# Optimization experiments

Hardware: AMD Instinct MI355X
Metric: run time of the kernel (lower is better)

## Reference

```python
import jax, jax.numpy as jnp
import numpy as np
import math

N_HEADS = 16
N_KV_HEADS = 4
D_HEAD = 128
EPS = 1e-6
THETA = 10000.0


def _rmsnorm(x, w):
    var = jnp.mean(x * x, axis=-1, keepdims=True)
    return x * jax.lax.rsqrt(var + EPS) * w


def _rope_tables(S, dtype):
    freqs = 1.0 / THETA ** (jnp.arange(0, D_HEAD, 2, dtype=jnp.float32) / D_HEAD)
    angles = jnp.arange(S, dtype=jnp.float32)[:, None] * freqs[None, :]  # [S, D_HEAD/2]
    angles = jnp.concatenate([angles, angles], axis=-1)  # [S, D_HEAD]
    return jnp.cos(angles).astype(dtype), jnp.sin(angles).astype(dtype)


def _apply_rope(x, cos, sin):
    # x: [B, H, S, D]; rotate-half convention matching cat([angles, angles])
    half = D_HEAD // 2
    x1, x2 = x[..., :half], x[..., half:]
    rot = jnp.concatenate([-x2, x1], axis=-1)
    return x * cos[None, None] + rot * sin[None, None]


def setup_inputs() -> dict:
    key = jax.random.key(0)
    ks = jax.random.split(key, 5)
    B, S, D = 2, 2048, 2048
    s = 0.02
    return {
        "x": jax.random.normal(ks[0], (B, S, D), jnp.float32),
        "Wq": jax.random.normal(ks[1], (D, N_HEADS * D_HEAD), jnp.float32) * s,
        "Wk": jax.random.normal(ks[2], (D, N_KV_HEADS * D_HEAD), jnp.float32) * s,
        "Wv": jax.random.normal(ks[3], (D, N_KV_HEADS * D_HEAD), jnp.float32) * s,
        "Wo": jax.random.normal(ks[4], (D, D), jnp.float32) * s,
        "q_norm_w": jnp.ones((D_HEAD,), jnp.float32),
        "k_norm_w": jnp.ones((D_HEAD,), jnp.float32),
    }


def reference(x, Wq, Wk, Wv, Wo, q_norm_w, k_norm_w):
    B, S, D = x.shape
    groups = N_HEADS // N_KV_HEADS

    q = (x @ Wq).reshape(B, S, N_HEADS, D_HEAD).transpose(0, 2, 1, 3)      # [B,H,S,d]
    k = (x @ Wk).reshape(B, S, N_KV_HEADS, D_HEAD).transpose(0, 2, 1, 3)   # [B,Hkv,S,d]
    v = (x @ Wv).reshape(B, S, N_KV_HEADS, D_HEAD).transpose(0, 2, 1, 3)

    q = _rmsnorm(q, q_norm_w)
    k = _rmsnorm(k, k_norm_w)

    cos, sin = _rope_tables(S, x.dtype)
    q = _apply_rope(q, cos, sin)
    k = _apply_rope(k, cos, sin)

    # GQA broadcast: repeat kv heads into query head dim
    k = jnp.repeat(k, groups, axis=1)  # [B,H,S,d]
    v = jnp.repeat(v, groups, axis=1)

    scale = 1.0 / math.sqrt(D_HEAD)
    scores = jnp.einsum("bhqd,bhkd->bhqk", q, k) * scale
    causal = jnp.tril(jnp.ones((S, S), bool))
    scores = jnp.where(causal[None, None], scores, jnp.finfo(scores.dtype).min)
    probs = jax.nn.softmax(scores, axis=-1)
    out = jnp.einsum("bhqk,bhkd->bhqd", probs, v)  # [B,H,S,d]
    out = out.transpose(0, 2, 1, 3).reshape(B, S, D)
    return out @ Wo
```

## Files before the change

kernel.cpp:

```cpp
#include <hip/hip_runtime.h>
#include <stdint.h>

typedef __attribute__((ext_vector_type(8))) short bf16x8;
typedef __attribute__((ext_vector_type(4))) float f32x4;
typedef unsigned short u16;
typedef unsigned int   u32;

#define S_LEN 2048
#define NH    16
#define NKV   4
#define DH    128
#define DM    2048
#define QKV_N 3072
#define MROWS 4096

__device__ __forceinline__ u16 f2bf(float x) {
  u32 u = __float_as_uint(x);
  return (u16)((u + 0x7fffu + ((u >> 16) & 1u)) >> 16);
}
__device__ __forceinline__ float bf2f(u16 h) {
  return __uint_as_float(((u32)h) << 16);
}
__device__ __forceinline__ u32 cvtpk(float lo, float hi) {
  u32 r;
  asm("v_cvt_pk_bf16_f32 %0, %1, %2" : "=v"(r) : "v"(lo), "v"(hi));
  return r;
}
__device__ __forceinline__ void gload_lds16(const void* g, void* l) {
  __builtin_amdgcn_global_load_lds((const __attribute__((address_space(1))) void*)g,
                                   (__attribute__((address_space(3))) void*)l, 16, 0, 0);
}

__global__ void __launch_bounds__(256) convert_x_kernel(const float* __restrict__ x,
                                                        u16* __restrict__ o) {
  int idx = (blockIdx.x * 256 + threadIdx.x) * 8;
  float4 a = *(const float4*)(x + idx);
  float4 b = *(const float4*)(x + idx + 4);
  union { u16 s[8]; uint4 v; } t;
  t.s[0] = f2bf(a.x); t.s[1] = f2bf(a.y); t.s[2] = f2bf(a.z); t.s[3] = f2bf(a.w);
  t.s[4] = f2bf(b.x); t.s[5] = f2bf(b.y); t.s[6] = f2bf(b.z); t.s[7] = f2bf(b.w);
  *(uint4*)(o + idx) = t.v;
}

__global__ void __launch_bounds__(256) transpose_w_kernel(const float* __restrict__ src,
                                                          u16* __restrict__ dst, int N) {
  __shared__ float t[64][65];
  const int bx = blockIdx.x, by = blockIdx.y, tid = threadIdx.x;
#pragma unroll
  for (int rep = 0; rep < 16; ++rep) {
    int lin = rep * 256 + tid;
    int i = lin >> 6, jj = lin & 63;
    t[i][jj] = src[(size_t)(bx * 64 + i) * N + by * 64 + jj];
  }
  __syncthreads();
#pragma unroll
  for (int rep = 0; rep < 16; ++rep) {
    int lin = rep * 256 + tid;
    int nr = lin >> 6, kc = lin & 63;
    dst[(size_t)(by * 64 + nr) * DM + bx * 64 + kc] = f2bf(t[kc][nr]);
  }
}

__global__ void __launch_bounds__(256) rope_tables_kernel(float* __restrict__ ct,
                                                          float* __restrict__ st_) {
  int idx = blockIdx.x * 256 + threadIdx.x;
  int s = idx >> 6, i = idx & 63;
  const float L2_10000 = 13.287712379549449f;
  float freq = exp2f(-(float)i * (1.0f / 64.0f) * L2_10000);
  float ang = (float)s * freq;
  ct[idx] = cosf(ang);
  st_[idx] = sinf(ang);
}

template <int OUTF32>
__global__ void __launch_bounds__(256) gemm_bt(const u16* __restrict__ A,
                                               const u16* __restrict__ Bt,
                                               void* __restrict__ C,
                                               int M, int N, int K) {
  __shared__ __align__(16) u16 As[128 * 32];
  __shared__ __align__(16) u16 Bs[128 * 32];
  const int tid = threadIdx.x;
  const int w = tid >> 6, l = tid & 63;
  const int g = l >> 4, q15 = l & 15;
  const int row0 = blockIdx.y * 128, col0 = blockIdx.x * 128;
  const int wm = (w >> 1) * 64, wn = (w & 1) * 64;
  const f32x4 fz = {0.f, 0.f, 0.f, 0.f};
  f32x4 acc[4][4];
#pragma unroll
  for (int m = 0; m < 4; ++m)
#pragma unroll
    for (int n = 0; n < 4; ++n) acc[m][n] = fz;

  for (int kt = 0; kt < K; kt += 32) {
#pragma unroll
    for (int c = 0; c < 2; ++c) {
      int P = (w * 2 + c) * 1024;
      int Pl = P + l * 16;
      int arow = Pl >> 6, acolb = Pl & 63;
      gload_lds16((const char*)A + ((size_t)(row0 + arow) * K + kt) * 2 + acolb,
                  (char*)As + P);
      gload_lds16((const char*)Bt + ((size_t)(col0 + arow) * K + kt) * 2 + acolb,
                  (char*)Bs + P);
    }
    __syncthreads();
    bf16x8 af[4], bfv[4];
#pragma unroll
    for (int m = 0; m < 4; ++m)
      af[m] = *(const bf16x8*)((const char*)As + (wm + m * 16 + q15) * 64 + g * 16);
#pragma unroll
    for (int n = 0; n < 4; ++n)
      bfv[n] = *(const bf16x8*)((const char*)Bs + (wn + n * 16 + q15) * 64 + g * 16);
#pragma unroll
    for (int m = 0; m < 4; ++m)
#pragma unroll
      for (int n = 0; n < 4; ++n)
        acc[m][n] = __builtin_amdgcn_mfma_f32_16x16x32_bf16(af[m], bfv[n], acc[m][n], 0, 0, 0);
    __syncthreads();
  }
#pragma unroll
  for (int m = 0; m < 4; ++m)
#pragma unroll
    for (int n = 0; n < 4; ++n)
#pragma unroll
      for (int r = 0; r < 4; ++r) {
        int rr = row0 + wm + m * 16 + g * 4 + r;
        int cc = col0 + wn + n * 16 + q15;
        float v = acc[m][n][r];
        if (OUTF32) ((float*)C)[(size_t)rr * N + cc] = v;
        else        ((u16*)C)[(size_t)rr * N + cc]  = f2bf(v);
      }
}

__global__ void __launch_bounds__(256) norm_rope_kernel(const u16* __restrict__ qkv,
                                                        const float* __restrict__ qw,
                                                        const float* __restrict__ kw,
                                                        const float* __restrict__ ct,
                                                        const float* __restrict__ st_,
                                                        u16* __restrict__ Qo,
                                                        u16* __restrict__ Ko) {
  int wid = blockIdx.x * 4 + (threadIdx.x >> 6);
  int l = threadIdx.x & 63;
  int row = wid / 20;
  int j = wid - row * 20;
  int b = row >> 11, s = row & 2047;
  bool isq = j < 16;
  int h = isq ? j : (j - 16);
  const u16* src = qkv + (size_t)row * QKV_N + (isq ? h * DH : (2048 + h * DH));
  float x1 = bf2f(src[l]), x2 = bf2f(src[l + 64]);
  float ss = x1 * x1 + x2 * x2;
#pragma unroll
  for (int off = 32; off > 0; off >>= 1) ss += __shfl_xor(ss, off);
  float rn = rsqrtf(ss * (1.0f / 128.0f) + 1e-6f);
  const float* wv = isq ? qw : kw;
  float n1 = x1 * rn * wv[l], n2 = x2 * rn * wv[l + 64];
  float cv = ct[s * 64 + l], sv = st_[s * 64 + l];
  float o1 = n1 * cv - n2 * sv;
  float o2 = n2 * cv + n1 * sv;
  float scale = isq ? 0.08838834764831845f : 1.0f;
  u16* dst = isq ? (Qo + ((size_t)(b * NH + h) * S_LEN + s) * DH)
                 : (Ko + ((size_t)(b * NKV + h) * S_LEN + s) * DH);
  dst[l]      = f2bf(o1 * scale);
  dst[l + 64] = f2bf(o2 * scale);
}

__global__ void __launch_bounds__(256) vtrans_kernel(const u16* __restrict__ qkv,
                                                     u16* __restrict__ vt) {
  __shared__ u16 t[64][65];
  const int st = blockIdx.x, dt = blockIdx.y, bz = blockIdx.z;
  const int tid = threadIdx.x;
#pragma unroll
  for (int rep = 0; rep < 16; ++rep) {
    int lin = rep * 256 + tid;
    int i = lin >> 6, jj = lin & 63;
    t[i][jj] = qkv[(size_t)((bz >> 2) * S_LEN + st * 64 + i) * QKV_N
                   + 2560 + (bz & 3) * DH + dt * 64 + jj];
  }
  __syncthreads();
#pragma unroll
  for (int rep = 0; rep < 16; ++rep) {
    int lin = rep * 256 + tid;
    int dr = lin >> 6, sc = lin & 63;
    vt[((size_t)bz * DH + dt * 64 + dr) * S_LEN + st * 64 + sc] = t[sc][dr];
  }
}

__global__ void __launch_bounds__(512, 4) attn_kernel(const u16* __restrict__ Qg,
                                                      const u16* __restrict__ Kg,
                                                      const u16* __restrict__ Vt,
                                                      u16* __restrict__ O) {
  __shared__ __align__(16) char smem[65536];
  const int tid = threadIdx.x;
  const int w = tid >> 6, l = tid & 63;
  const int g = l >> 4, q15 = l & 15;
  const int id = blockIdx.x;
  const int grp = id & 7;
  const int mem = (id >> 3) & 3;
  const int tq  = 15 - (id >> 5);
  const int b   = grp >> 2, kvh = grp & 3;
  const int h   = kvh * 4 + mem;
  const int qb  = tq * 128;
  const int nkt = 2 * tq + 1;

  bf16x8 qreg[4];
  const u16* Qrow = Qg + ((size_t)(b * NH + h) * S_LEN + qb + w * 16 + q15) * DH;
#pragma unroll
  for (int c = 0; c < 4; ++c)
    qreg[c] = *(const bf16x8*)(Qrow + c * 32 + g * 8);

  const char* Kbase = (const char*)(Kg + (size_t)(b * NKV + kvh) * S_LEN * DH);
  const char* Vbase = (const char*)(Vt + (size_t)(b * NKV + kvh) * DH * S_LEN);

  auto stage = [&](int buf, int kt) {
    char* Ksb = smem + buf * 32768;
    if (w < 4) {
      const char* Kt = Kbase + (size_t)kt * 64 * 256;
#pragma unroll
      for (int i = 0; i < 4; ++i) {
        int off = w * 4096 + i * 1024 + l * 16;
        int row = off >> 8; int cb = (off & 255) ^ ((row & 7) << 4);
        gload_lds16(Kt + (size_t)row * 256 + cb, Ksb + off);
      }
    } else {
      const char* Vtb = Vbase + (size_t)kt * 128;
      char* Vsb = Ksb + 16384;
#pragma unroll
      for (int i = 0; i < 4; ++i) {
        int off = (w - 4) * 4096 + i * 1024 + l * 16;
        int row = off >> 7; int cb = (off & 127) ^ ((row & 7) << 4);
        gload_lds16(Vtb + (size_t)row * (S_LEN * 2) + cb, Vsb + off);
      }
    }
  };

  const f32x4 fz = {0.f, 0.f, 0.f, 0.f};
  f32x4 acc[8];
#pragma unroll
  for (int n = 0; n < 8; ++n) acc[n] = fz;
  float mrun = -1e30f, lrun = 0.f;

  stage(0, 0);
  __syncthreads();
  int cur = 0;

  for (int kt = 0; kt <= nkt; ++kt) {
    if (kt < nkt) stage(cur ^ 1, kt + 1);
    const char* Ks = smem + cur * 32768;
    const char* Vs = Ks + 16384;

    f32x4 sa[4];
#pragma unroll
    for (int stt = 0; stt < 4; ++stt) sa[stt] = fz;
    __builtin_amdgcn_s_setprio(1);
#pragma unroll
    for (int stt = 0; stt < 4; ++stt) {
      int krow = stt * 16 + q15;
      const char* kr = Ks + krow * 256;
      int sw = (krow & 7) << 4;
#pragma unroll
      for (int c = 0; c < 4; ++c) {
        bf16x8 kf = *(const bf16x8*)(kr + ((c * 64 + g * 16) ^ sw));
        sa[stt] = __builtin_amdgcn_mfma_f32_16x16x32_bf16(kf, qreg[c], sa[stt], 0, 0, 0);
      }
    }
    __builtin_amdgcn_s_setprio(0);

    const bool domask = (kt >= 2 * tq);
    float tmax = -1e30f;
#pragma unroll
    for (int stt = 0; stt < 4; ++stt)
#pragma unroll
      for (int r = 0; r < 4; ++r) {
        float v = sa[stt][r];
        if (domask) {
          int kvg = kt * 64 + stt * 16 + g * 4 + r;
          int qg  = qb + w * 16 + q15;
          if (kvg > qg) v = -1e30f;
        }
        sa[stt][r] = v;
        tmax = fmaxf(tmax, v);
      }
    tmax = fmaxf(tmax, __shfl_xor(tmax, 16));
    tmax = fmaxf(tmax, __shfl_xor(tmax, 32));

    const bool defer = __all(tmax <= mrun + 8.0f);
    float mnew = defer ? mrun : fmaxf(mrun, tmax);

    float tsum = 0.f;
    u32 pk[4][2];
#pragma unroll
    for (int stt = 0; stt < 4; ++stt) {
      float p0 = __expf(sa[stt][0] - mnew);
      float p1 = __expf(sa[stt][1] - mnew);
      float p2 = __expf(sa[stt][2] - mnew);
      float p3 = __expf(sa[stt][3] - mnew);
      tsum += p0 + p1 + p2 + p3;
      pk[stt][0] = cvtpk(p0, p1);
      pk[stt][1] = cvtpk(p2, p3);
    }
    tsum += __shfl_xor(tsum, 16);
    tsum += __shfl_xor(tsum, 32);

    if (defer) {
      lrun += tsum;
    } else {
      float alpha = __expf(mrun - mnew);
      lrun = lrun * alpha + tsum;
      mrun = mnew;
      float af4[4];
#pragma unroll
      for (int r = 0; r < 4; ++r) af4[r] = __shfl(alpha, g * 4 + r);
#pragma unroll
      for (int n = 0; n < 8; ++n) {
        f32x4 t = acc[n];
        t[0] *= af4[0]; t[1] *= af4[1]; t[2] *= af4[2]; t[3] *= af4[3];
        acc[n] = t;
      }
    }

#pragma unroll
    for (int c = 0; c < 2; ++c) {
      int srcA = ((2 * (g & 1)) << 4) | q15;
      int srcB = srcA + 16;
      u32 a00 = __shfl(pk[2 * c][0], srcA),     a01 = __shfl(pk[2 * c][1], srcA);
      u32 a02 = __shfl(pk[2 * c][0], srcB),     a03 = __shfl(pk[2 * c][1], srcB);
      u32 a10 = __shfl(pk[2 * c + 1][0], srcA), a11 = __shfl(pk[2 * c + 1][1], srcA);
      u32 a12 = __shfl(pk[2 * c + 1][0], srcB), a13 = __shfl(pk[2 * c + 1][1], srcB);
      bool hi = (g & 2) != 0;
      union { u32 u[4]; bf16x8 v; } afr;
      afr.u[0] = hi ? a10 : a00;
      afr.u[1] = hi ? a11 : a01;
      afr.u[2] = hi ? a12 : a02;
      afr.u[3] = hi ? a13 : a03;
      __builtin_amdgcn_s_setprio(1);
#pragma unroll
      for (int n = 0; n < 8; ++n) {
        int d = n * 16 + q15;
        const char* vr = Vs + d * 128;
        int sw = (d & 7) << 4;
        bf16x8 bv = *(const bf16x8*)(vr + ((c * 64 + g * 16) ^ sw));
        acc[n] = __builtin_amdgcn_mfma_f32_16x16x32_bf16(afr.v, bv, acc[n], 0, 0, 0);
      }
      __builtin_amdgcn_s_setprio(0);
    }
    __syncthreads();
    cur ^= 1;
  }

  float linv[4];
#pragma unroll
  for (int r = 0; r < 4; ++r) linv[r] = 1.0f / __shfl(lrun, g * 4 + r);
#pragma unroll
  for (int n = 0; n < 8; ++n)
#pragma unroll
    for (int r = 0; r < 4; ++r) {
      size_t orow = (size_t)b * S_LEN + qb + w * 16 + g * 4 + r;
      O[orow * DM + h * DH + n * 16 + q15] = f2bf(acc[n][r] * linv[r]);
    }
}

extern "C" void kernel_launch(void* const* d_in, const int* in_sizes, int n_in,
                              void* d_out, int out_size, void* d_ws, size_t ws_size,
                              hipStream_t stream) {
  (void)in_sizes; (void)n_in; (void)out_size; (void)ws_size;
  const float* x  = (const float*)d_in[0];
  const float* Wq = (const float*)d_in[1];
  const float* Wk = (const float*)d_in[2];
  const float* Wv = (const float*)d_in[3];
  const float* Wo = (const float*)d_in[4];
  const float* qw = (const float*)d_in[5];
  const float* kw = (const float*)d_in[6];

  char* ws = (char*)d_ws;
  u16*   xb    = (u16*)(ws + 0);
  u16*   wqkvt = (u16*)(ws + 16777216);
  u16*   wot   = (u16*)(ws + 29360128);
  u16*   qo    = (u16*)(ws + 37748736);
  u16*   ko    = (u16*)(ws + 54525952);
  u16*   vt    = (u16*)(ws + 58720256);
  float* ctab  = (float*)(ws + 62914560);
  float* stab  = (float*)(ws + 63438848);
  u16*   qkvp  = (u16*)d_out;
  u16*   attn  = (u16*)(ws + 0);
  float* outp  = (float*)d_out;

  convert_x_kernel<<<4096, 256, 0, stream>>>(x, xb);
  transpose_w_kernel<<<dim3(32, 32), 256, 0, stream>>>(Wq, wqkvt, 2048);
  transpose_w_kernel<<<dim3(32, 8),  256, 0, stream>>>(Wk, wqkvt + (size_t)2048 * 2048, 512);
  transpose_w_kernel<<<dim3(32, 8),  256, 0, stream>>>(Wv, wqkvt + (size_t)2560 * 2048, 512);
  transpose_w_kernel<<<dim3(32, 32), 256, 0, stream>>>(Wo, wot, 2048);
  rope_tables_kernel<<<512, 256, 0, stream>>>(ctab, stab);

  gemm_bt<0><<<dim3(24, 32), 256, 0, stream>>>(xb, wqkvt, qkvp, MROWS, QKV_N, DM);
  norm_rope_kernel<<<20480, 256, 0, stream>>>(qkvp, qw, kw, ctab, stab, qo, ko);
  vtrans_kernel<<<dim3(32, 2, 8), 256, 0, stream>>>(qkvp, vt);
  attn_kernel<<<512, 512, 0, stream>>>(qo, ko, vt, attn);
  gemm_bt<1><<<dim3(16, 32), 256, 0, stream>>>(attn, wot, outp, MROWS, DM, DM);
}
```

Baseline: 254.7 us.

## Process two 16-row query tiles per wave in attention, halving block threads

```diff
diff --git a/kernel.cpp b/kernel.cpp
--- a/kernel.cpp
+++ b/kernel.cpp
@@ -184,7 +184,7 @@
   }
 }
 
-__global__ void __launch_bounds__(512, 4) attn_kernel(const u16* __restrict__ Qg,
+__global__ void __launch_bounds__(256, 2) attn_kernel(const u16* __restrict__ Qg,
                                                       const u16* __restrict__ Kg,
                                                       const u16* __restrict__ Vt,
                                                       u16* __restrict__ O) {
@@ -201,42 +201,40 @@
   const int qb  = tq * 128;
   const int nkt = 2 * tq + 1;
 
-  bf16x8 qreg[4];
-  const u16* Qrow = Qg + ((size_t)(b * NH + h) * S_LEN + qb + w * 16 + q15) * DH;
-#pragma unroll
-  for (int c = 0; c < 4; ++c)
-    qreg[c] = *(const bf16x8*)(Qrow + c * 32 + g * 8);
+  bf16x8 qreg[2][4];
+#pragma unroll
+  for (int p = 0; p < 2; ++p) {
+    const u16* Qrow = Qg + ((size_t)(b * NH + h) * S_LEN + qb + w * 32 + p * 16 + q15) * DH;
+#pragma unroll
+    for (int c = 0; c < 4; ++c)
+      qreg[p][c] = *(const bf16x8*)(Qrow + c * 32 + g * 8);
+  }
 
   const char* Kbase = (const char*)(Kg + (size_t)(b * NKV + kvh) * S_LEN * DH);
   const char* Vbase = (const char*)(Vt + (size_t)(b * NKV + kvh) * DH * S_LEN);
 
   auto stage = [&](int buf, int kt) {
     char* Ksb = smem + buf * 32768;
-    if (w < 4) {
-      const char* Kt = Kbase + (size_t)kt * 64 * 256;
-#pragma unroll
-      for (int i = 0; i < 4; ++i) {
-        int off = w * 4096 + i * 1024 + l * 16;
-        int row = off >> 8; int cb = (off & 255) ^ ((row & 7) << 4);
-        gload_lds16(Kt + (size_t)row * 256 + cb, Ksb + off);
-      }
-    } else {
-      const char* Vtb = Vbase + (size_t)kt * 128;
-      char* Vsb = Ksb + 16384;
-#pragma unroll
-      for (int i = 0; i < 4; ++i) {
-        int off = (w - 4) * 4096 + i * 1024 + l * 16;
-        int row = off >> 7; int cb = (off & 127) ^ ((row & 7) << 4);
-        gload_lds16(Vtb + (size_t)row * (S_LEN * 2) + cb, Vsb + off);
-      }
+    char* Vsb = Ksb + 16384;
+    const char* Kt  = Kbase + (size_t)kt * 64 * 256;
+    const char* Vtb = Vbase + (size_t)kt * 128;
+#pragma unroll
+    for (int i = 0; i < 4; ++i) {
+      int off = w * 4096 + i * 1024 + l * 16;
+      { int row = off >> 8; int cb = (off & 255) ^ ((row & 7) << 4);
+        gload_lds16(Kt + (size_t)row * 256 + cb, Ksb + off); }
+      { int row = off >> 7; int cb = (off & 127) ^ ((row & 7) << 4);
+        gload_lds16(Vtb + (size_t)row * (S_LEN * 2) + cb, Vsb + off); }
     }
   };
 
   const f32x4 fz = {0.f, 0.f, 0.f, 0.f};
-  f32x4 acc[8];
-#pragma unroll
-  for (int n = 0; n < 8; ++n) acc[n] = fz;
-  float mrun = -1e30f, lrun = 0.f;
+  f32x4 acc[2][8];
+#pragma unroll
+  for (int p = 0; p < 2; ++p)
+#pragma unroll
+    for (int n = 0; n < 8; ++n) acc[p][n] = fz;
+  float mrun[2] = {-1e30f, -1e30f}, lrun[2] = {0.f, 0.f};
 
   stage(0, 0);
   __syncthreads();
@@ -247,9 +245,11 @@
     const char* Ks = smem + cur * 32768;
     const char* Vs = Ks + 16384;
 
-    f32x4 sa[4];
-#pragma unroll
-    for (int stt = 0; stt < 4; ++stt) sa[stt] = fz;
+    f32x4 sa[2][4];
+#pragma unroll
+    for (int p = 0; p < 2; ++p)
+#pragma unroll
+      for (int stt = 0; stt < 4; ++stt) sa[p][stt] = fz;
     __builtin_amdgcn_s_setprio(1);
 #pragma unroll
     for (int stt = 0; stt < 4; ++stt) {
@@ -259,61 +259,67 @@
 #pragma unroll
       for (int c = 0; c < 4; ++c) {
         bf16x8 kf = *(const bf16x8*)(kr + ((c * 64 + g * 16) ^ sw));
-        sa[stt] = __builtin_amdgcn_mfma_f32_16x16x32_bf16(kf, qreg[c], sa[stt], 0, 0, 0);
+        sa[0][stt] = __builtin_amdgcn_mfma_f32_16x16x32_bf16(kf, qreg[0][c], sa[0][stt], 0, 0, 0);
+        sa[1][stt] = __builtin_amdgcn_mfma_f32_16x16x32_bf16(kf, qreg[1][c], sa[1][stt], 0, 0, 0);
       }
     }
     __builtin_amdgcn_s_setprio(0);
 
-    const bool domask = (kt >= 2 * tq);
-    float tmax = -1e30f;
-#pragma unroll
-    for (int stt = 0; stt < 4; ++stt)
-#pragma unroll
-      for (int r = 0; r < 4; ++r) {
-        float v = sa[stt][r];
-        if (domask) {
-          int kvg = kt * 64 + stt * 16 + g * 4 + r;
-          int qg  = qb + w * 16 + q15;
-          if (kvg > qg) v = -1e30f;
+    float tmax[2] = {-1e30f, -1e30f};
+#pragma unroll
+    for (int p = 0; p < 2; ++p) {
+      const bool domask = (kt * 64 + 63) > (qb + w * 32 + p * 16);
+#pragma unroll
+      for (int stt = 0; stt < 4; ++stt)
+#pragma unroll
+        for (int r = 0; r < 4; ++r) {
+          float v = sa[p][stt][r];
+          if (domask) {
+            int kvg = kt * 64 + stt * 16 + g * 4 + r;
+            int qg  = qb + w * 32 + p * 16 + q15;
+            if (kvg > qg) v = -1e30f;
+          }
+          sa[p][stt][r] = v;
+          tmax[p] = fmaxf(tmax[p], v);
         }
-        sa[stt][r] = v;
-        tmax = fmaxf(tmax, v);
-      }
-    tmax = fmaxf(tmax, __shfl_xor(tmax, 16));
-    tmax = fmaxf(tmax, __shfl_xor(tmax, 32));
-
-    const bool defer = __all(tmax <= mrun + 8.0f);
-    float mnew = defer ? mrun : fmaxf(mrun, tmax);
-
-    float tsum = 0.f;
-    u32 pk[4][2];
-#pragma unroll
-    for (int stt = 0; stt < 4; ++stt) {
-      float p0 = __expf(sa[stt][0] - mnew);
-      float p1 = __expf(sa[stt][1] - mnew);
-      float p2 = __expf(sa[stt][2] - mnew);
-      float p3 = __expf(sa[stt][3] - mnew);
-      tsum += p0 + p1 + p2 + p3;
-      pk[stt][0] = cvtpk(p0, p1);
-      pk[stt][1] = cvtpk(p2, p3);
-    }
-    tsum += __shfl_xor(tsum, 16);
-    tsum += __shfl_xor(tsum, 32);
-
-    if (defer) {
-      lrun += tsum;
-    } else {
-      float alpha = __expf(mrun - mnew);
-      lrun = lrun * alpha + tsum;
-      mrun = mnew;
-      float af4[4];
-#pragma unroll
-      for (int r = 0; r < 4; ++r) af4[r] = __shfl(alpha, g * 4 + r);
-#pragma unroll
-      for (int n = 0; n < 8; ++n) {
-        f32x4 t = acc[n];
-        t[0] *= af4[0]; t[1] *= af4[1]; t[2] *= af4[2]; t[3] *= af4[3];
-        acc[n] = t;
+      tmax[p] = fmaxf(tmax[p], __shfl_xor(tmax[p], 16));
+      tmax[p] = fmaxf(tmax[p], __shfl_xor(tmax[p], 32));
+    }
+
+    const bool defer = __all(tmax[0] <= mrun[0] + 8.0f && tmax[1] <= mrun[1] + 8.0f);
+
+    u32 pk[2][4][2];
+#pragma unroll
+    for (int p = 0; p < 2; ++p) {
+      float mnew = defer ? mrun[p] : fmaxf(mrun[p], tmax[p]);
+      float tsum = 0.f;
+#pragma unroll
+      for (int stt = 0; stt < 4; ++stt) {
+        float p0 = __expf(sa[p][stt][0] - mnew);
+        float p1 = __expf(sa[p][stt][1] - mnew);
+        float p2 = __expf(sa[p][stt][2] - mnew);
+        float p3 = __expf(sa[p][stt][3] - mnew);
+        tsum += p0 + p1 + p2 + p3;
+        pk[p][stt][0] = cvtpk(p0, p1);
+        pk[p][stt][1] = cvtpk(p2, p3);
+      }
+      tsum += __shfl_xor(tsum, 16);
+      tsum += __shfl_xor(tsum, 32);
+      if (defer) {
+        lrun[p] += tsum;
+      } else {
+        float alpha = __expf(mrun[p] - mnew);
+        lrun[p] = lrun[p] * alpha + tsum;
+        mrun[p] = mnew;
+        float af4[4];
+#pragma unroll
+        for (int r = 0; r < 4; ++r) af4[r] = __shfl(alpha, g * 4 + r);
+#pragma unroll
+        for (int n = 0; n < 8; ++n) {
+          f32x4 t = acc[p][n];
+          t[0] *= af4[0]; t[1] *= af4[1]; t[2] *= af4[2]; t[3] *= af4[3];
+          acc[p][n] = t;
+        }
       }
     }
 
@@ -321,16 +327,19 @@
     for (int c = 0; c < 2; ++c) {
       int srcA = ((2 * (g & 1)) << 4) | q15;
       int srcB = srcA + 16;
-      u32 a00 = __shfl(pk[2 * c][0], srcA),     a01 = __shfl(pk[2 * c][1], srcA);
-      u32 a02 = __shfl(pk[2 * c][0], srcB),     a03 = __shfl(pk[2 * c][1], srcB);
-      u32 a10 = __shfl(pk[2 * c + 1][0], srcA), a11 = __shfl(pk[2 * c + 1][1], srcA);
-      u32 a12 = __shfl(pk[2 * c + 1][0], srcB), a13 = __shfl(pk[2 * c + 1][1], srcB);
-      bool hi = (g & 2) != 0;
-      union { u32 u[4]; bf16x8 v; } afr;
-      afr.u[0] = hi ? a10 : a00;
-      afr.u[1] = hi ? a11 : a01;
-      afr.u[2] = hi ? a12 : a02;
-      afr.u[3] = hi ? a13 : a03;
+      union { u32 u[4]; bf16x8 v; } afr[2];
+#pragma unroll
+      for (int p = 0; p < 2; ++p) {
+        u32 a00 = __shfl(pk[p][2 * c][0], srcA),     a01 = __shfl(pk[p][2 * c][1], srcA);
+        u32 a02 = __shfl(pk[p][2 * c][0], srcB),     a03 = __shfl(pk[p][2 * c][1], srcB);
+        u32 a10 = __shfl(pk[p][2 * c + 1][0], srcA), a11 = __shfl(pk[p][2 * c + 1][1], srcA);
+        u32 a12 = __shfl(pk[p][2 * c + 1][0], srcB), a13 = __shfl(pk[p][2 * c + 1][1], srcB);
+        bool hi = (g & 2) != 0;
+        afr[p].u[0] = hi ? a10 : a00;
+        afr[p].u[1] = hi ? a11 : a01;
+        afr[p].u[2] = hi ? a12 : a02;
+        afr[p].u[3] = hi ? a13 : a03;
+      }
       __builtin_amdgcn_s_setprio(1);
 #pragma unroll
       for (int n = 0; n < 8; ++n) {
@@ -338,7 +347,8 @@
         const char* vr = Vs + d * 128;
         int sw = (d & 7) << 4;
         bf16x8 bv = *(const bf16x8*)(vr + ((c * 64 + g * 16) ^ sw));
-        acc[n] = __builtin_amdgcn_mfma_f32_16x16x32_bf16(afr.v, bv, acc[n], 0, 0, 0);
+        acc[0][n] = __builtin_amdgcn_mfma_f32_16x16x32_bf16(afr[0].v, bv, acc[0][n], 0, 0, 0);
+        acc[1][n] = __builtin_amdgcn_mfma_f32_16x16x32_bf16(afr[1].v, bv, acc[1][n], 0, 0, 0);
       }
       __builtin_amdgcn_s_setprio(0);
     }
@@ -346,16 +356,19 @@
     cur ^= 1;
   }
 
-  float linv[4];
-#pragma unroll
-  for (int r = 0; r < 4; ++r) linv[r] = 1.0f / __shfl(lrun, g * 4 + r);
-#pragma unroll
-  for (int n = 0; n < 8; ++n)
-#pragma unroll
-    for (int r = 0; r < 4; ++r) {
-      size_t orow = (size_t)b * S_LEN + qb + w * 16 + g * 4 + r;
-      O[orow * DM + h * DH + n * 16 + q15] = f2bf(acc[n][r] * linv[r]);
-    }
+#pragma unroll
+  for (int p = 0; p < 2; ++p) {
+    float linv[4];
+#pragma unroll
+    for (int r = 0; r < 4; ++r) linv[r] = 1.0f / __shfl(lrun[p], g * 4 + r);
+#pragma unroll
+    for (int n = 0; n < 8; ++n)
+#pragma unroll
+      for (int r = 0; r < 4; ++r) {
+        size_t orow = (size_t)b * S_LEN + qb + w * 32 + p * 16 + g * 4 + r;
+        O[orow * DM + h * DH + n * 16 + q15] = f2bf(acc[p][n][r] * linv[r]);
+      }
+  }
 }
 
 extern "C" void kernel_launch(void* const* d_in, const int* in_sizes, int n_in,
@@ -393,6 +406,6 @@
   gemm_bt<0><<<dim3(24, 32), 256, 0, stream>>>(xb, wqkvt, qkvp, MROWS, QKV_N, DM);
   norm_rope_kernel<<<20480, 256, 0, stream>>>(qkvp, qw, kw, ctab, stab, qo, ko);
   vtrans_kernel<<<dim3(32, 2, 8), 256, 0, stream>>>(qkvp, vt);
-  attn_kernel<<<512, 512, 0, stream>>>(qo, ko, vt, attn);
+  attn_kernel<<<512, 256, 0, stream>>>(qo, ko, vt, attn);
   gemm_bt<1><<<dim3(16, 32), 256, 0, stream>>>(attn, wot, outp, MROWS, DM, DM);
 }
```

Result: slower. 261.1 us (+2.5%).

## Switch attention to 32x32x16 MFMA with 4 waves of 32 query rows

Applied to the files above, without the earlier changes.

```diff
diff --git a/kernel.cpp b/kernel.cpp
--- a/kernel.cpp
+++ b/kernel.cpp
@@ -3,8 +3,10 @@
 
 typedef __attribute__((ext_vector_type(8))) short bf16x8;
 typedef __attribute__((ext_vector_type(4))) float f32x4;
+typedef __attribute__((ext_vector_type(16))) float f32x16;
 typedef unsigned short u16;
 typedef unsigned int   u32;
+typedef unsigned long long u64;
 
 #define S_LEN 2048
 #define NH    16
@@ -25,6 +27,9 @@
   u32 r;
   asm("v_cvt_pk_bf16_f32 %0, %1, %2" : "=v"(r) : "v"(lo), "v"(hi));
   return r;
+}
+__device__ __forceinline__ void plswap(u32& a, u32& b) {
+  asm volatile("v_permlane32_swap_b32 %0, %1" : "+v"(a), "+v"(b));
 }
 __device__ __forceinline__ void gload_lds16(const void* g, void* l) {
   __builtin_amdgcn_global_load_lds((const __attribute__((address_space(1))) void*)g,
@@ -184,14 +189,14 @@
   }
 }
 
-__global__ void __launch_bounds__(512, 4) attn_kernel(const u16* __restrict__ Qg,
+__global__ void __launch_bounds__(256, 2) attn_kernel(const u16* __restrict__ Qg,
                                                       const u16* __restrict__ Kg,
                                                       const u16* __restrict__ Vt,
                                                       u16* __restrict__ O) {
   __shared__ __align__(16) char smem[65536];
   const int tid = threadIdx.x;
   const int w = tid >> 6, l = tid & 63;
-  const int g = l >> 4, q15 = l & 15;
+  const int q31 = l & 31, hi = l >> 5;
   const int id = blockIdx.x;
   const int grp = id & 7;
   const int mem = (id >> 3) & 3;
@@ -200,42 +205,42 @@
   const int h   = kvh * 4 + mem;
   const int qb  = tq * 128;
   const int nkt = 2 * tq + 1;
-
-  bf16x8 qreg[4];
-  const u16* Qrow = Qg + ((size_t)(b * NH + h) * S_LEN + qb + w * 16 + q15) * DH;
-#pragma unroll
-  for (int c = 0; c < 4; ++c)
-    qreg[c] = *(const bf16x8*)(Qrow + c * 32 + g * 8);
+  const int qg  = qb + w * 32 + q31;
+
+  bf16x8 qreg[8];
+  const u16* Qrow = Qg + ((size_t)(b * NH + h) * S_LEN + qg) * DH;
+#pragma unroll
+  for (int c = 0; c < 8; ++c)
+    qreg[c] = *(const bf16x8*)(Qrow + c * 16 + hi * 8);
 
   const char* Kbase = (const char*)(Kg + (size_t)(b * NKV + kvh) * S_LEN * DH);
   const char* Vbase = (const char*)(Vt + (size_t)(b * NKV + kvh) * DH * S_LEN);
 
   auto stage = [&](int buf, int kt) {
     char* Ksb = smem + buf * 32768;
-    if (w < 4) {
-      const char* Kt = Kbase + (size_t)kt * 64 * 256;
-#pragma unroll
-      for (int i = 0; i < 4; ++i) {
-        int off = w * 4096 + i * 1024 + l * 16;
-        int row = off >> 8; int cb = (off & 255) ^ ((row & 7) << 4);
-        gload_lds16(Kt + (size_t)row * 256 + cb, Ksb + off);
-      }
-    } else {
-      const char* Vtb = Vbase + (size_t)kt * 128;
-      char* Vsb = Ksb + 16384;
-#pragma unroll
-      for (int i = 0; i < 4; ++i) {
-        int off = (w - 4) * 4096 + i * 1024 + l * 16;
-        int row = off >> 7; int cb = (off & 127) ^ ((row & 7) << 4);
-        gload_lds16(Vtb + (size_t)row * (S_LEN * 2) + cb, Vsb + off);
-      }
+    char* Vsb = Ksb + 16384;
+    const char* Kt  = Kbase + (size_t)kt * 64 * 256;
+    const char* Vtb = Vbase + (size_t)kt * 128;
+#pragma unroll
+    for (int i = 0; i < 4; ++i) {
+      int off = w * 4096 + i * 1024 + l * 16;
+      int row = off >> 8;
+      {
+        int cb = (off & 255) ^ ((row & 15) << 4);
+        gload_lds16(Kt + (size_t)row * 256 + cb, Ksb + off); }
+      {
+        int qoff = (off & 255) ^ ((row & 15) << 4);
+        int d = row * 2 + (qoff >> 7);
+        int kvb = qoff & 127;
+        gload_lds16(Vtb + (size_t)d * (S_LEN * 2) + kvb, Vsb + off); }
     }
   };
 
-  const f32x4 fz = {0.f, 0.f, 0.f, 0.f};
-  f32x4 acc[8];
-#pragma unroll
-  for (int n = 0; n < 8; ++n) acc[n] = fz;
+  f32x16 acc[4];
+#pragma unroll
+  for (int dt = 0; dt < 4; ++dt)
+#pragma unroll
+    for (int r = 0; r < 16; ++r) acc[dt][r] = 0.f;
   float mrun = -1e30f, lrun = 0.f;
 
   stage(0, 0);
@@ -247,57 +252,66 @@
     const char* Ks = smem + cur * 32768;
     const char* Vs = Ks + 16384;
 
-    f32x4 sa[4];
-#pragma unroll
-    for (int stt = 0; stt < 4; ++stt) sa[stt] = fz;
+    f32x16 sa[2];
+#pragma unroll
+    for (int s = 0; s < 2; ++s)
+#pragma unroll
+      for (int r = 0; r < 16; ++r) sa[s][r] = 0.f;
     __builtin_amdgcn_s_setprio(1);
 #pragma unroll
-    for (int stt = 0; stt < 4; ++stt) {
-      int krow = stt * 16 + q15;
+    for (int s = 0; s < 2; ++s) {
+      int krow = s * 32 + q31;
       const char* kr = Ks + krow * 256;
-      int sw = (krow & 7) << 4;
-#pragma unroll
-      for (int c = 0; c < 4; ++c) {
-        bf16x8 kf = *(const bf16x8*)(kr + ((c * 64 + g * 16) ^ sw));
-        sa[stt] = __builtin_amdgcn_mfma_f32_16x16x32_bf16(kf, qreg[c], sa[stt], 0, 0, 0);
+      int sw = (krow & 15) << 4;
+#pragma unroll
+      for (int c = 0; c < 8; ++c) {
+        bf16x8 kf = *(const bf16x8*)(kr + ((c * 32 + hi * 16) ^ sw));
+        sa[s] = __builtin_amdgcn_mfma_f32_32x32x16_bf16(kf, qreg[c], sa[s], 0, 0, 0);
       }
     }
     __builtin_amdgcn_s_setprio(0);
 
-    const bool domask = (kt >= 2 * tq);
+    const bool domask = (kt * 64 + 63) > (qb + w * 32);
     float tmax = -1e30f;
 #pragma unroll
-    for (int stt = 0; stt < 4; ++stt)
-#pragma unroll
-      for (int r = 0; r < 4; ++r) {
-        float v = sa[stt][r];
+    for (int s = 0; s < 2; ++s)
+#pragma unroll
+      for (int r = 0; r < 16; ++r) {
+        float v = sa[s][r];
         if (domask) {
-          int kvg = kt * 64 + stt * 16 + g * 4 + r;
-          int qg  = qb + w * 16 + q15;
+          int kvg = kt * 64 + s * 32 + (r & 3) + 8 * (r >> 2) + 4 * hi;
           if (kvg > qg) v = -1e30f;
         }
-        sa[stt][r] = v;
+        sa[s][r] = v;
         tmax = fmaxf(tmax, v);
       }
-    tmax = fmaxf(tmax, __shfl_xor(tmax, 16));
     tmax = fmaxf(tmax, __shfl_xor(tmax, 32));
 
     const bool defer = __all(tmax <= mrun + 8.0f);
-    float mnew = defer ? mrun : fmaxf(mrun, tmax);
+    const float mnew = defer ? mrun : fmaxf(mrun, tmax);
 
     float tsum = 0.f;
-    u32 pk[4][2];
-#pragma unroll
-    for (int stt = 0; stt < 4; ++stt) {
-      float p0 = __expf(sa[stt][0] - mnew);
-      float p1 = __expf(sa[stt][1] - mnew);
-      float p2 = __expf(sa[stt][2] - mnew);
-      float p3 = __expf(sa[stt][3] - mnew);
-      tsum += p0 + p1 + p2 + p3;
-      pk[stt][0] = cvtpk(p0, p1);
-      pk[stt][1] = cvtpk(p2, p3);
-    }
-    tsum += __shfl_xor(tsum, 16);
+    union { u32 u[4]; bf16x8 v; } pf[4];
+#pragma unroll
+    for (int s = 0; s < 2; ++s)
+#pragma unroll
+      for (int kl = 0; kl < 2; ++kl) {
+        float e0 = __expf(sa[s][kl * 8 + 0] - mnew);
+        float e1 = __expf(sa[s][kl * 8 + 1] - mnew);
+        float e2 = __expf(sa[s][kl * 8 + 2] - mnew);
+        float e3 = __expf(sa[s][kl * 8 + 3] - mnew);
+        float e4 = __expf(sa[s][kl * 8 + 4] - mnew);
+        float e5 = __expf(sa[s][kl * 8 + 5] - mnew);
+        float e6 = __expf(sa[s][kl * 8 + 6] - mnew);
+        float e7 = __expf(sa[s][kl * 8 + 7] - mnew);
+        tsum += (e0 + e1) + (e2 + e3) + (e4 + e5) + (e6 + e7);
+        u32 A0 = cvtpk(e0, e1), A1 = cvtpk(e2, e3);
+        u32 B0 = cvtpk(e4, e5), B1 = cvtpk(e6, e7);
+        plswap(A0, B0);
+        plswap(A1, B1);
+        int ks = s * 2 + kl;
+        pf[ks].u[0] = A0; pf[ks].u[1] = A1; pf[ks].u[2] = B0; pf[ks].u[3] = B1;
+      }
     tsum += __shfl_xor(tsum, 32);
 
     if (defer) {
@@ -306,55 +320,43 @@
       float alpha = __expf(mrun - mnew);
       lrun = lrun * alpha + tsum;
       mrun = mnew;
-      float af4[4];
-#pragma unroll
-      for (int r = 0; r < 4; ++r) af4[r] = __shfl(alpha, g * 4 + r);
-#pragma unroll
-      for (int n = 0; n < 8; ++n) {
-        f32x4 t = acc[n];
-        t[0] *= af4[0]; t[1] *= af4[1]; t[2] *= af4[2]; t[3] *= af4[3];
-        acc[n] = t;
+#pragma unroll
+      for (int dt = 0; dt < 4; ++dt)
+#pragma unroll
+        for (int r = 0; r < 16; ++r) acc[dt][r] *= alpha;
+    }
+
+    __builtin_amdgcn_s_setprio(1);
+#pragma unroll
+    for (int dt = 0; dt < 4; ++dt) {
+      int d = dt * 32 + q31;
+      int vrow = d >> 1;
+      const char* vr = Vs + vrow * 256;
+      int sw = (vrow & 15) << 4;
+      int hb = (d & 1) << 7;
+#pragma unroll
+      for (int ks = 0; ks < 4; ++ks) {
+        bf16x8 vf = *(const bf16x8*)(vr + ((hb | (ks * 32 + hi * 16)) ^ sw));
+        acc[dt] = __builtin_amdgcn_mfma_f32_32x32x16_bf16(vf, pf[ks].v, acc[dt], 0, 0, 0);
       }
     }
-
-#pragma unroll
-    for (int c = 0; c < 2; ++c) {
-      int srcA = ((2 * (g & 1)) << 4) | q15;
-      int srcB = srcA + 16;
-      u32 a00 = __shfl(pk[2 * c][0], srcA),     a01 = __shfl(pk[2 * c][1], srcA);
-      u32 a02 = __shfl(pk[2 * c][0], srcB),     a03 = __shfl(pk[2 * c][1], srcB);
-      u32 a10 = __shfl(pk[2 * c + 1][0], srcA), a11 = __shfl(pk[2 * c + 1][1], srcA);
-      u32 a12 = __shfl(pk[2 * c + 1][0], srcB), a13 = __shfl(pk[2 * c + 1][1], srcB);
-      bool hi = (g & 2) != 0;
-      union { u32 u[4]; bf16x8 v; } afr;
-      afr.u[0] = hi ? a10 : a00;
-      afr.u[1] = hi ? a11 : a01;
-      afr.u[2] = hi ? a12 : a02;
-      afr.u[3] = hi ? a13 : a03;
-      __builtin_amdgcn_s_setprio(1);
-#pragma unroll
-      for (int n = 0; n < 8; ++n) {
-        int d = n * 16 + q15;
-        const char* vr = Vs + d * 128;
-        int sw = (d & 7) << 4;
-        bf16x8 bv = *(const bf16x8*)(vr + ((c * 64 + g * 16) ^ sw));
-        acc[n] = __builtin_amdgcn_mfma_f32_16x16x32_bf16(afr.v, bv, acc[n], 0, 0, 0);
-      }
-      __builtin_amdgcn_s_setprio(0);
-    }
+    __builtin_amdgcn_s_setprio(0);
+
     __syncthreads();
     cur ^= 1;
   }
 
-  float linv[4];
-#pragma unroll
-  for (int r = 0; r < 4; ++r) linv[r] = 1.0f / __shfl(lrun, g * 4 + r);
-#pragma unroll
-  for (int n = 0; n < 8; ++n)
-#pragma unroll
-    for (int r = 0; r < 4; ++r) {
-      size_t orow = (size_t)b * S_LEN + qb + w * 16 + g * 4 + r;
-      O[orow * DM + h * DH + n * 16 + q15] = f2bf(acc[n][r] * linv[r]);
+  const float linv = 1.0f / lrun;
+  u16* Obase = O + ((size_t)b * S_LEN + qg) * DM + h * DH;
+#pragma unroll
+  for (int dt = 0; dt < 4; ++dt)
+#pragma unroll
+    for (int rg = 0; rg < 4; ++rg) {
+      int d0 = dt * 32 + rg * 8 + hi * 4;
+      u32 w0 = cvtpk(acc[dt][rg * 4 + 0] * linv, acc[dt][rg * 4 + 1] * linv);
+      u32 w1 = cvtpk(acc[dt][rg * 4 + 2] * linv, acc[dt][rg * 4 + 3] * linv);
+      u64 vv = (u64)w0 | ((u64)w1 << 32);
+      *(u64*)(Obase + d0) = vv;
     }
 }
 
@@ -393,6 +395,6 @@
   gemm_bt<0><<<dim3(24, 32), 256, 0, stream>>>(xb, wqkvt, qkvp, MROWS, QKV_N, DM);
   norm_rope_kernel<<<20480, 256, 0, stream>>>(qkvp, qw, kw, ctab, stab, qo, ko);
   vtrans_kernel<<<dim3(32, 2, 8), 256, 0, stream>>>(qkvp, vt);
-  attn_kernel<<<512, 512, 0, stream>>>(qo, ko, vt, attn);
+  attn_kernel<<<512, 256, 0, stream>>>(qo, ko, vt, attn);
   gemm_bt<1><<<dim3(16, 32), 256, 0, stream>>>(attn, wot, outp, MROWS, DM, DM);
 }
```

New measurement: 240.1 us. 5.7% less time.
